# Optimization experiments

Measured on AMD Instinct MI355X. Metric: run time of the kernel, lower is better.

The kernel has to match this reference:

```python
import jax, jax.numpy as jnp
import numpy as np

BETA = 0.25


def setup_inputs() -> dict:
    key = jax.random.key(0)
    k1, k2 = jax.random.split(key)
    inputs = jax.random.normal(k1, (16, 32, 32, 256), dtype=jnp.float32)
    codebook = jax.random.normal(k2, (8192, 256), dtype=jnp.float32)
    return {"inputs": inputs, "codebook": codebook}


def reference(inputs, codebook):
    sg = jax.lax.stop_gradient
    latent_size = inputs.shape[-1]
    flat = inputs.reshape(-1, latent_size)  # [N, C]
    d = (jnp.sum(flat ** 2, axis=1, keepdims=True)
         + jnp.sum(codebook ** 2, axis=1)
         - 2.0 * flat @ codebook.T)
    min_encoding_indices = jnp.argmin(d, axis=1)  # [N]
    z_q = codebook[min_encoding_indices].reshape(inputs.shape)
    loss = (jnp.mean((sg(z_q) - inputs) ** 2)
            + BETA * jnp.mean((z_q - sg(inputs)) ** 2))
    z_q_st = inputs + sg(z_q - inputs)  # straight-through estimator
    return (z_q_st, loss, min_encoding_indices)
```

## Files before the change

kernel.cpp:

```cpp
#include <hip/hip_runtime.h>

#define M_ROWS 16384
#define N_CODES 8192
#define K_DIM   256
#define NSPLIT  16
#define SCAP    16384
#define TAU     0.05f

typedef _Float16 half8 __attribute__((ext_vector_type(8)));
typedef float floatx16 __attribute__((ext_vector_type(16)));

#define GLL16(g, l) __builtin_amdgcn_global_load_lds(                         \
    (const __attribute__((address_space(1))) void*)(g),                       \
    (__attribute__((address_space(3))) void*)(l), 16, 0, 0)

#define MFMA16(a, b, c) __builtin_amdgcn_mfma_f32_32x32x16_f16(a, b, c, 0, 0, 0)
#define SCB __builtin_amdgcn_sched_barrier(0)

__global__ void pack_all(const float* __restrict__ x, const float* __restrict__ cb,
                         _Float16* __restrict__ Apack, _Float16* __restrict__ Bpack,
                         float* __restrict__ en2, int* __restrict__ cntS) {
  const int bid = blockIdx.x;
  const int tid = threadIdx.x;
  if (bid == 0 && tid < NSPLIT) cntS[tid] = 0;
  if (bid < 1024) {
    const int t = bid * 256 + tid;
    const int C = t >> 5, G = t & 31;
    const int ct = C >> 5, r32 = C & 31;
    const int kc = G >> 2, g2 = G & 3, ks = g2 >> 1, lh = g2 & 1;
    const float* src = cb + (size_t)C * K_DIM + G * 8;
    half8 hv;
    float ss = 0.f;
#pragma unroll
    for (int j = 0; j < 8; ++j) {
      const float v = src[j];
      hv[j] = (_Float16)v;
      ss += v * v;
    }
    ss += __shfl_xor(ss, 1, 32); ss += __shfl_xor(ss, 2, 32);
    ss += __shfl_xor(ss, 4, 32); ss += __shfl_xor(ss, 8, 32);
    ss += __shfl_xor(ss, 16, 32);
    if (G == 0) en2[C] = 0.5f * ss;
    _Float16* blob = Apack + ((size_t)ct * 8 + kc) * 1024;
    const int off = ((ks * 2 + lh) * 32 + r32) * 8;
    *reinterpret_cast<half8*>(blob + off) = hv;
  } else {
    const int t = (bid - 1024) * 256 + tid;
    const int R = t >> 5, G = t & 31;
    const int rt = R >> 7, r = R & 127, jt = r >> 5, rr = r & 31;
    const int kc = G >> 2, g2 = G & 3, ks = g2 >> 1, lh = g2 & 1;
    const float* src = x + (size_t)R * K_DIM + G * 8;
    half8 hv;
#pragma unroll
    for (int j = 0; j < 8; ++j) hv[j] = (_Float16)src[j];
    _Float16* blob = Bpack + ((size_t)rt * 8 + kc) * 4096;
    const int off = ((jt * 2 + ks) * 2 + lh) * 256 + rr * 8;
    *reinterpret_cast<half8*>(blob + off) = hv;
  }
}

__global__ __launch_bounds__(256, 2)
void vq_dist(const _Float16* __restrict__ Apack, const _Float16* __restrict__ Bpack,
             const float* __restrict__ en2, float* __restrict__ candV,
             int* __restrict__ candI, float* __restrict__ cand2) {
  __shared__ _Float16 ldsB[32768];

  const int tid = threadIdx.x;
  const int wv = tid >> 6, lane = tid & 63;
  const int l31 = lane & 31, lh = lane >> 5;

  const int lid = blockIdx.x;
  const int xcd = lid & 7, q = lid >> 3;
  const int cs = xcd >> 1;
  const int bx = q * 2 + (xcd & 1);

  const _Float16* gB = Bpack + (size_t)bx * 32768;
#pragma unroll
  for (int s = 0; s < 16; ++s)
    GLL16(gB + (s * 256 + tid) * 8, ldsB + (s * 256 + tid) * 8);

  const int tbase = (cs * 4 + wv) * 16;
  half8 a[2][2][2];
  {
    const _Float16* gA0 = Apack + ((size_t)tbase) * 8192;
#pragma unroll
    for (int it = 0; it < 2; ++it)
#pragma unroll
      for (int ks = 0; ks < 2; ++ks)
        a[0][it][ks] = *reinterpret_cast<const half8*>(
            gA0 + (size_t)it * 8192 + ((ks * 2 + lh) * 32 + l31) * 8);
  }

  asm volatile("s_waitcnt vmcnt(4)" ::: "memory");
  SCB;
  __builtin_amdgcn_s_barrier();
  SCB;

  float b1[4] = {-3.0e38f, -3.0e38f, -3.0e38f, -3.0e38f};
  float b2[4] = {-3.0e38f, -3.0e38f, -3.0e38f, -3.0e38f};
  int i1[4] = {0, 0, 0, 0};

  for (int c = 0; c < 8; ++c) {
    const int t0 = tbase + c * 2;
    floatx16 acc[2][4] = {};
#pragma unroll
    for (int kc = 0; kc < 8; ++kc) {
      const int par = kc & 1, npar = par ^ 1;
      if (!(c == 7 && kc == 7)) {
        const int nt0 = (kc < 7) ? t0 : (t0 + 2);
        const int nkc = (kc < 7) ? (kc + 1) : 0;
        const _Float16* gA = Apack + ((size_t)nt0 * 8 + nkc) * 1024;
#pragma unroll
        for (int it = 0; it < 2; ++it)
#pragma unroll
          for (int ks = 0; ks < 2; ++ks)
            a[npar][it][ks] = *reinterpret_cast<const half8*>(
                gA + (size_t)it * 8192 + ((ks * 2 + lh) * 32 + l31) * 8);
      }
      SCB;
      half8 b[4][2];
#pragma unroll
      for (int jt = 0; jt < 4; ++jt)
#pragma unroll
        for (int ks = 0; ks < 2; ++ks)
          b[jt][ks] = *reinterpret_cast<const half8*>(
              ldsB + kc * 4096 + ((jt * 2 + ks) * 2 + lh) * 256 + l31 * 8);
      __builtin_amdgcn_s_setprio(1);
#pragma unroll
      for (int ks = 0; ks < 2; ++ks)
#pragma unroll
        for (int it = 0; it < 2; ++it)
#pragma unroll
          for (int jt = 0; jt < 4; ++jt)
            acc[it][jt] = MFMA16(a[par][it][ks], b[jt][ks], acc[it][jt]);
      __builtin_amdgcn_s_setprio(0);
    }

#pragma unroll
    for (int it = 0; it < 2; ++it) {
      const int code0 = (t0 + it) * 32;
      const float* ep = en2 + code0 + 4 * lh;
      const float4 e0 = *reinterpret_cast<const float4*>(ep);
      const float4 e1 = *reinterpret_cast<const float4*>(ep + 8);
      const float4 e2 = *reinterpret_cast<const float4*>(ep + 16);
      const float4 e3 = *reinterpret_cast<const float4*>(ep + 24);
      const float ev[16] = {e0.x, e0.y, e0.z, e0.w, e1.x, e1.y, e1.z, e1.w,
                            e2.x, e2.y, e2.z, e2.w, e3.x, e3.y, e3.z, e3.w};
#pragma unroll
      for (int reg = 0; reg < 16; ++reg) {
        const int code = code0 + (reg & 3) + 8 * (reg >> 2) + 4 * lh;
#pragma unroll
        for (int jt = 0; jt < 4; ++jt) {
          const float v = acc[it][jt][reg] - ev[reg];
          b2[jt] = fmaxf(b2[jt], fminf(v, b1[jt]));
          i1[jt] = (v > b1[jt]) ? code : i1[jt];
          b1[jt] = fmaxf(b1[jt], v);
        }
      }
    }
  }

#pragma unroll
  for (int jt = 0; jt < 4; ++jt) {
    const float o1 = __shfl_xor(b1[jt], 32, 64);
    const int oi = __shfl_xor(i1[jt], 32, 64);
    const float o2 = __shfl_xor(b2[jt], 32, 64);
    const float lose = fminf(b1[jt], o1);
    i1[jt] = (b1[jt] >= o1) ? i1[jt] : oi;
    b1[jt] = fmaxf(b1[jt], o1);
    b2[jt] = fmaxf(fmaxf(b2[jt], o2), lose);
  }

  if (lane < 32) {
    const int split = cs * 4 + wv;
#pragma unroll
    for (int jt = 0; jt < 4; ++jt) {
      const int row = bx * 128 + jt * 32 + l31;
      candV[(size_t)split * M_ROWS + row] = b1[jt];
      candI[(size_t)split * M_ROWS + row] = i1[jt];
      cand2[(size_t)split * M_ROWS + row] = b2[jt];
    }
  }
}

__global__ void vq_reduce(const float* __restrict__ candV, const int* __restrict__ candI,
                          const float* __restrict__ cand2, int* __restrict__ cntS,
                          int* __restrict__ riskyS, unsigned long long* __restrict__ key) {
  const int row = blockIdx.x * 256 + threadIdx.x;
  float v[NSPLIT];
#pragma unroll
  for (int s = 0; s < NSPLIT; ++s) v[s] = candV[(size_t)s * M_ROWS + row];
  float b1 = v[0];
  int i1 = candI[row];
  float b2 = cand2[row];
#pragma unroll
  for (int s = 1; s < NSPLIT; ++s) {
    const int ii = candI[(size_t)s * M_ROWS + row];
    const float v2 = cand2[(size_t)s * M_ROWS + row];
    const float lose = fminf(b1, v[s]);
    i1 = (v[s] > b1) ? ii : i1;
    b1 = fmaxf(b1, v[s]);
    b2 = fmaxf(fmaxf(b2, v2), lose);
  }
  if (b1 - b2 < TAU) {
    key[row] = 0ull;
    const float thr = b1 - TAU;
#pragma unroll
    for (int s = 0; s < NSPLIT; ++s) {
      if (v[s] > thr) {
        const int p = atomicAdd(&cntS[s], 1);
        riskyS[(size_t)s * SCAP + p] = row;
      }
    }
  } else {
    unsigned u = __float_as_uint(b1);
    u ^= (u >> 31) ? 0xFFFFFFFFu : 0x80000000u;
    key[row] = ((unsigned long long)u << 32) | (unsigned)(N_CODES - 1 - i1);
  }
}

__global__ __launch_bounds__(256)
void vq_refine(const float* __restrict__ x, const float* __restrict__ cb,
               const float* __restrict__ en2, const int* __restrict__ cntS,
               const int* __restrict__ riskyS, unsigned long long* __restrict__ key) {
  __shared__ float cbs[32][260];
  __shared__ float xs[8][260];
  __shared__ int rowS[8];
  const int split = blockIdx.x >> 4;
  const int n = cntS[split];
  if (n == 0) return;
  const int tid = threadIdx.x;
  const int cBase = split * 512 + (blockIdx.x & 15) * 32;
  const int* list = riskyS + (size_t)split * SCAP;
  const int cl = tid >> 3, rs = tid & 7;
#pragma unroll
  for (int q = 0; q < 32; ++q) cbs[q][tid] = cb[(size_t)(cBase + q) * K_DIM + tid];
  const float e_c = en2[cBase + cl];
  for (int t0 = blockIdx.y * 8; t0 < n; t0 += 16) {
    __syncthreads();
    if (tid < 8) {
      const int ti = t0 + tid;
      rowS[tid] = list[ti < n ? ti : n - 1];
    }
    __syncthreads();
#pragma unroll
    for (int r = 0; r < 8; ++r) xs[r][tid] = x[(size_t)rowS[r] * K_DIM + tid];
    __syncthreads();
    float s0 = 0.f, s1 = 0.f;
#pragma unroll 4
    for (int k4 = 0; k4 < 64; k4 += 2) {
      const float4 c0 = *reinterpret_cast<const float4*>(&cbs[cl][k4 * 4]);
      const float4 x0 = *reinterpret_cast<const float4*>(&xs[rs][k4 * 4]);
      const float4 c1 = *reinterpret_cast<const float4*>(&cbs[cl][k4 * 4 + 4]);
      const float4 x1 = *reinterpret_cast<const float4*>(&xs[rs][k4 * 4 + 4]);
      s0 = fmaf(x0.x, c0.x, s0); s0 = fmaf(x0.y, c0.y, s0);
      s0 = fmaf(x0.z, c0.z, s0); s0 = fmaf(x0.w, c0.w, s0);
      s1 = fmaf(x1.x, c1.x, s1); s1 = fmaf(x1.y, c1.y, s1);
      s1 = fmaf(x1.z, c1.z, s1); s1 = fmaf(x1.w, c1.w, s1);
    }
    const float sc = (s0 + s1) - e_c;
    unsigned u = __float_as_uint(sc);
    u ^= (u >> 31) ? 0xFFFFFFFFu : 0x80000000u;
    unsigned long long k64 =
        ((unsigned long long)u << 32) | (unsigned)(N_CODES - 1 - (cBase + cl));
    {
      unsigned long long o;
      o = __shfl_xor(k64, 8, 64);  if (o > k64) k64 = o;
      o = __shfl_xor(k64, 16, 64); if (o > k64) k64 = o;
      o = __shfl_xor(k64, 32, 64); if (o > k64) k64 = o;
    }
    if (((tid >> 3) & 7) == 0) atomicMax(key + rowS[rs], k64);
  }
}

__global__ void vq_gather(const float* __restrict__ x, const float* __restrict__ cb,
                          const unsigned long long* __restrict__ key, float* __restrict__ zq,
                          float* __restrict__ idxf, float* __restrict__ partial) {
  __shared__ float red[256];
  const int g = blockIdx.x * 256 + threadIdx.x;
  const int row = g >> 6;
  const int c4 = g & 63;
  const int idx = N_CODES - 1 - (int)(unsigned)(key[row] & 0xFFFFFFFFull);
  if (c4 == 0) idxf[row] = (float)idx;
  const float4 z = *reinterpret_cast<const float4*>(cb + (size_t)idx * K_DIM + c4 * 4);
  const float4 xv = *reinterpret_cast<const float4*>(x + (size_t)g * 4);
  *reinterpret_cast<float4*>(zq + (size_t)g * 4) = z;
  const float dx = z.x - xv.x, dy = z.y - xv.y, dz = z.z - xv.z, dw = z.w - xv.w;
  red[threadIdx.x] = dx * dx + dy * dy + dz * dz + dw * dw;
  __syncthreads();
  for (int o = 128; o > 0; o >>= 1) {
    if (threadIdx.x < o) red[threadIdx.x] += red[threadIdx.x + o];
    __syncthreads();
  }
  if (threadIdx.x == 0) partial[blockIdx.x] = red[0];
}

__global__ void vq_loss(const float* __restrict__ partial, float* __restrict__ out) {
  __shared__ float red[256];
  float s = 0.f;
  for (int i = threadIdx.x; i < 4096; i += 256) s += partial[i];
  red[threadIdx.x] = s;
  __syncthreads();
  for (int o = 128; o > 0; o >>= 1) {
    if (threadIdx.x < o) red[threadIdx.x] += red[threadIdx.x + o];
    __syncthreads();
  }
  if (threadIdx.x == 0) out[0] = 1.25f * red[0] / 4194304.0f;
}

extern "C" void kernel_launch(void* const* d_in, const int* in_sizes, int n_in,
                              void* d_out, int out_size, void* d_ws, size_t ws_size,
                              hipStream_t stream) {
  const float* x = (const float*)d_in[0];
  const float* cb = (const float*)d_in[1];
  float* out = (float*)d_out;
  float* zq = out;
  float* loss = out + 4194304;
  float* idxf = out + 4194305;

  char* w = (char*)d_ws;
  _Float16* Apack = (_Float16*)w;                      w += (size_t)N_CODES * K_DIM * 2;
  _Float16* Bpack = (_Float16*)w;                      w += (size_t)M_ROWS * K_DIM * 2;
  unsigned long long* key = (unsigned long long*)w;    w += (size_t)M_ROWS * 8;
  float* en2 = (float*)w;                              w += (size_t)N_CODES * 4;
  float* candV = (float*)w;                            w += (size_t)M_ROWS * NSPLIT * 4;
  float* cand2 = (float*)w;                            w += (size_t)M_ROWS * NSPLIT * 4;
  int* candI = (int*)w;                                w += (size_t)M_ROWS * NSPLIT * 4;
  int* riskyS = (int*)w;                               w += (size_t)NSPLIT * SCAP * 4;
  int* cntS = (int*)w;                                 w += 64;
  float* part = (float*)w;                             w += 4096 * 4;

  pack_all<<<3072, 256, 0, stream>>>(x, cb, Apack, Bpack, en2, cntS);
  vq_dist<<<512, 256, 0, stream>>>(Apack, Bpack, en2, candV, candI, cand2);
  vq_reduce<<<M_ROWS / 256, 256, 0, stream>>>(candV, candI, cand2, cntS, riskyS, key);
  vq_refine<<<dim3(256, 2), 256, 0, stream>>>(x, cb, en2, cntS, riskyS, key);
  vq_gather<<<4194304 / (256 * 4), 256, 0, stream>>>(x, cb, key, zq, idxf, part);
  vq_loss<<<1, 256, 0, stream>>>(part, loss);
}
```

Measured before the change: 121.6 us.

## Double vq_dist rows per block so wave pairs share codebook tiles

vq_dist now runs 512-thread blocks that stage 256 input rows in LDS instead of 128. Each pair of waves streams the same codebook tiles but works on different row halves. Waves 4-7 start at a staggered codebook chunk, so a block's global A traffic is shared across more rows. The Bpack layout in pack_all is changed to match, and both pack paths now use float4 loads. The en2 bias is folded into the accumulator init, which takes a subtraction out of the argmin epilogue. The catch is 128KB of LDS per block, which limits residency to one block per CU.

```diff
diff --git a/kernel.cpp b/kernel.cpp
--- a/kernel.cpp
+++ b/kernel.cpp
@@ -29,13 +29,15 @@
     const int ct = C >> 5, r32 = C & 31;
     const int kc = G >> 2, g2 = G & 3, ks = g2 >> 1, lh = g2 & 1;
     const float* src = cb + (size_t)C * K_DIM + G * 8;
+    const float4 v0 = *reinterpret_cast<const float4*>(src);
+    const float4 v1 = *reinterpret_cast<const float4*>(src + 4);
+    const float vv[8] = {v0.x, v0.y, v0.z, v0.w, v1.x, v1.y, v1.z, v1.w};
     half8 hv;
     float ss = 0.f;
 #pragma unroll
     for (int j = 0; j < 8; ++j) {
-      const float v = src[j];
-      hv[j] = (_Float16)v;
-      ss += v * v;
+      hv[j] = (_Float16)vv[j];
+      ss += vv[j] * vv[j];
     }
     ss += __shfl_xor(ss, 1, 32); ss += __shfl_xor(ss, 2, 32);
     ss += __shfl_xor(ss, 4, 32); ss += __shfl_xor(ss, 8, 32);
@@ -47,42 +49,48 @@
   } else {
     const int t = (bid - 1024) * 256 + tid;
     const int R = t >> 5, G = t & 31;
-    const int rt = R >> 7, r = R & 127, jt = r >> 5, rr = r & 31;
+    const int rt = R >> 8, r = R & 255, rg = r >> 5, rr = r & 31;
     const int kc = G >> 2, g2 = G & 3, ks = g2 >> 1, lh = g2 & 1;
     const float* src = x + (size_t)R * K_DIM + G * 8;
+    const float4 v0 = *reinterpret_cast<const float4*>(src);
+    const float4 v1 = *reinterpret_cast<const float4*>(src + 4);
     half8 hv;
-#pragma unroll
-    for (int j = 0; j < 8; ++j) hv[j] = (_Float16)src[j];
-    _Float16* blob = Bpack + ((size_t)rt * 8 + kc) * 4096;
-    const int off = ((jt * 2 + ks) * 2 + lh) * 256 + rr * 8;
+    hv[0] = (_Float16)v0.x; hv[1] = (_Float16)v0.y;
+    hv[2] = (_Float16)v0.z; hv[3] = (_Float16)v0.w;
+    hv[4] = (_Float16)v1.x; hv[5] = (_Float16)v1.y;
+    hv[6] = (_Float16)v1.z; hv[7] = (_Float16)v1.w;
+    _Float16* blob = Bpack + (size_t)rt * 65536;
+    const int off = (((kc * 8 + rg) * 4 + ks * 2 + lh) * 32 + rr) * 8;
     *reinterpret_cast<half8*>(blob + off) = hv;
   }
 }
 
-__global__ __launch_bounds__(256, 2)
+__global__ __launch_bounds__(512, 2)
 void vq_dist(const _Float16* __restrict__ Apack, const _Float16* __restrict__ Bpack,
              const float* __restrict__ en2, float* __restrict__ candV,
              int* __restrict__ candI, float* __restrict__ cand2) {
-  __shared__ _Float16 ldsB[32768];
+  __shared__ _Float16 ldsB[65536];
 
   const int tid = threadIdx.x;
   const int wv = tid >> 6, lane = tid & 63;
   const int l31 = lane & 31, lh = lane >> 5;
+  const int g = wv >> 1, h = wv & 1;
+  const int coff = wv & 4;
 
   const int lid = blockIdx.x;
   const int xcd = lid & 7, q = lid >> 3;
   const int cs = xcd >> 1;
   const int bx = q * 2 + (xcd & 1);
 
-  const _Float16* gB = Bpack + (size_t)bx * 32768;
+  const _Float16* gB = Bpack + (size_t)bx * 65536;
 #pragma unroll
   for (int s = 0; s < 16; ++s)
-    GLL16(gB + (s * 256 + tid) * 8, ldsB + (s * 256 + tid) * 8);
-
-  const int tbase = (cs * 4 + wv) * 16;
+    GLL16(gB + (s * 512 + tid) * 8, ldsB + (s * 512 + tid) * 8);
+
+  const int tbase = (cs * 4 + g) * 16;
   half8 a[2][2][2];
   {
-    const _Float16* gA0 = Apack + ((size_t)tbase) * 8192;
+    const _Float16* gA0 = Apack + (size_t)(tbase + coff * 2) * 8192;
 #pragma unroll
     for (int it = 0; it < 2; ++it)
 #pragma unroll
@@ -101,13 +109,33 @@
   int i1[4] = {0, 0, 0, 0};
 
   for (int c = 0; c < 8; ++c) {
-    const int t0 = tbase + c * 2;
-    floatx16 acc[2][4] = {};
+    const int cc = (c + coff) & 7;
+    const int t0 = tbase + cc * 2;
+
+    floatx16 acc[2][4];
+#pragma unroll
+    for (int it = 0; it < 2; ++it) {
+      const float* ep = en2 + (t0 + it) * 32 + 4 * lh;
+      const float4 e0 = *reinterpret_cast<const float4*>(ep);
+      const float4 e1 = *reinterpret_cast<const float4*>(ep + 8);
+      const float4 e2 = *reinterpret_cast<const float4*>(ep + 16);
+      const float4 e3 = *reinterpret_cast<const float4*>(ep + 24);
+      const float ev[16] = {e0.x, e0.y, e0.z, e0.w, e1.x, e1.y, e1.z, e1.w,
+                            e2.x, e2.y, e2.z, e2.w, e3.x, e3.y, e3.z, e3.w};
+#pragma unroll
+      for (int reg = 0; reg < 16; ++reg) {
+        const float ne = -ev[reg];
+#pragma unroll
+        for (int jt = 0; jt < 4; ++jt) acc[it][jt][reg] = ne;
+      }
+    }
+
 #pragma unroll
     for (int kc = 0; kc < 8; ++kc) {
       const int par = kc & 1, npar = par ^ 1;
       if (!(c == 7 && kc == 7)) {
-        const int nt0 = (kc < 7) ? t0 : (t0 + 2);
+        const int ncc = (c + 1 + coff) & 7;
+        const int nt0 = (kc < 7) ? t0 : (tbase + ncc * 2);
         const int nkc = (kc < 7) ? (kc + 1) : 0;
         const _Float16* gA = Apack + ((size_t)nt0 * 8 + nkc) * 1024;
 #pragma unroll
@@ -124,7 +152,7 @@
 #pragma unroll
         for (int ks = 0; ks < 2; ++ks)
           b[jt][ks] = *reinterpret_cast<const half8*>(
-              ldsB + kc * 4096 + ((jt * 2 + ks) * 2 + lh) * 256 + l31 * 8);
+              ldsB + (((kc * 8 + h * 4 + jt) * 4 + ks * 2 + lh) * 32 + l31) * 8);
       __builtin_amdgcn_s_setprio(1);
 #pragma unroll
       for (int ks = 0; ks < 2; ++ks)
@@ -139,22 +167,16 @@
 #pragma unroll
     for (int it = 0; it < 2; ++it) {
       const int code0 = (t0 + it) * 32;
-      const float* ep = en2 + code0 + 4 * lh;
-      const float4 e0 = *reinterpret_cast<const float4*>(ep);
-      const float4 e1 = *reinterpret_cast<const float4*>(ep + 8);
-      const float4 e2 = *reinterpret_cast<const float4*>(ep + 16);
-      const float4 e3 = *reinterpret_cast<const float4*>(ep + 24);
-      const float ev[16] = {e0.x, e0.y, e0.z, e0.w, e1.x, e1.y, e1.z, e1.w,
-                            e2.x, e2.y, e2.z, e2.w, e3.x, e3.y, e3.z, e3.w};
 #pragma unroll
       for (int reg = 0; reg < 16; ++reg) {
         const int code = code0 + (reg & 3) + 8 * (reg >> 2) + 4 * lh;
 #pragma unroll
         for (int jt = 0; jt < 4; ++jt) {
-          const float v = acc[it][jt][reg] - ev[reg];
-          b2[jt] = fmaxf(b2[jt], fminf(v, b1[jt]));
+          const float v = acc[it][jt][reg];
+          const float t = fminf(v, b1[jt]);
           i1[jt] = (v > b1[jt]) ? code : i1[jt];
           b1[jt] = fmaxf(b1[jt], v);
+          b2[jt] = fmaxf(b2[jt], t);
         }
       }
     }
@@ -172,10 +194,10 @@
   }
 
   if (lane < 32) {
-    const int split = cs * 4 + wv;
+    const int split = cs * 4 + g;
 #pragma unroll
     for (int jt = 0; jt < 4; ++jt) {
-      const int row = bx * 128 + jt * 32 + l31;
+      const int row = bx * 256 + h * 128 + jt * 32 + l31;
       candV[(size_t)split * M_ROWS + row] = b1[jt];
       candI[(size_t)split * M_ROWS + row] = i1[jt];
       cand2[(size_t)split * M_ROWS + row] = b2[jt];
@@ -331,7 +353,7 @@
   float* part = (float*)w;                             w += 4096 * 4;
 
   pack_all<<<3072, 256, 0, stream>>>(x, cb, Apack, Bpack, en2, cntS);
-  vq_dist<<<512, 256, 0, stream>>>(Apack, Bpack, en2, candV, candI, cand2);
+  vq_dist<<<256, 512, 0, stream>>>(Apack, Bpack, en2, candV, candI, cand2);
   vq_reduce<<<M_ROWS / 256, 256, 0, stream>>>(candV, candI, cand2, cntS, riskyS, key);
   vq_refine<<<dim3(256, 2), 256, 0, stream>>>(x, cb, en2, cntS, riskyS, key);
   vq_gather<<<4194304 / (256 * 4), 256, 0, stream>>>(x, cb, key, zq, idxf, part);
```

New measurement: 125.2 us. 1.03x slower.
